# Kernel optimization log

Measured on AMD Instinct MI355X. Metric: run time of the kernel, lower is better.

The kernel has to match this reference:

```python
import jax, jax.numpy as jnp
import numpy as np

B, S, D = 4, 4096, 256

def setup_inputs() -> dict:
    key = jax.random.key(0)
    k1, k2, k3, k4 = jax.random.split(key, 4)
    inputs = jax.random.normal(k1, (B, S, D), dtype=jnp.float32)
    Wq = jax.random.normal(k2, (D, D), dtype=jnp.float32) * 0.05
    Wk = jax.random.normal(k3, (D, D), dtype=jnp.float32) * 0.05
    Wv = jax.random.normal(k4, (D, D), dtype=jnp.float32) * 0.05
    return {"inputs": inputs, "Wq": Wq, "Wk": Wk, "Wv": Wv}

def reference(inputs, Wq, Wk, Wv):
    # single-head self-attention: softmax(QK^T / sqrt(d)) V
    d = inputs.shape[-1]
    Q = jnp.einsum('bsd,de->bse', inputs, Wq)
    K = jnp.einsum('bsd,de->bse', inputs, Wk)
    V = jnp.einsum('bsd,de->bse', inputs, Wv)
    scale = 1.0 / jnp.sqrt(jnp.asarray(d, dtype=inputs.dtype))
    scores = jnp.einsum('bqe,bke->bqk', Q, K) * scale  # [B,S,S]
    attn = jax.nn.softmax(scores, axis=-1)
    return jnp.einsum('bqk,bke->bqe', attn, V)
```

## Files before the change

### kernel.cpp

```cpp
#include <hip/hip_runtime.h>
#include <hip/hip_bf16.h>

typedef __attribute__((ext_vector_type(8))) short bfrag_t;
typedef __attribute__((ext_vector_type(4))) float facc_t;
typedef __attribute__((ext_vector_type(16))) float f16acc_t;
typedef __attribute__((ext_vector_type(4))) int i4_t;

#define B_ 4
#define S_ 4096
#define D_ 256

using gas_v = const __attribute__((address_space(1))) void;
using las_v = __attribute__((address_space(3))) void;

__device__ __forceinline__ short f2bf(float f) {
  union { float fv; unsigned u; } x; x.fv = f;
  unsigned r = x.u + 0x7FFFu + ((x.u >> 16) & 1u);
  return (short)(r >> 16);
}

__device__ __forceinline__ int cvtpk(float lo, float hi) {
  int r;
  asm("v_cvt_pk_bf16_f32 %0, %1, %2" : "=v"(r) : "v"(lo), "v"(hi));
  return r;
}

__device__ __forceinline__ facc_t mfma16(bfrag_t a, bfrag_t b, facc_t c) {
  return __builtin_amdgcn_mfma_f32_16x16x32_bf16(a, b, c, 0, 0, 0);
}
__device__ __forceinline__ f16acc_t mfma32(bfrag_t a, bfrag_t b, f16acc_t c) {
  return __builtin_amdgcn_mfma_f32_32x32x16_bf16(a, b, c, 0, 0, 0);
}

__global__ void wt_kernel(const float* __restrict__ Wq, const float* __restrict__ Wk,
                          const float* __restrict__ Wv, short* __restrict__ WT) {
  const int p = blockIdx.x >> 4;
  const float* W = (p == 0) ? Wq : ((p == 1) ? Wk : Wv);
  short* o = WT + p * (D_ * D_);
  const int e = (blockIdx.x & 15) * 16 + (threadIdx.x >> 4);
  const int td = threadIdx.x & 15;
  #pragma unroll
  for (int dd = 0; dd < 16; ++dd) {
    int d = td * 16 + dd;
    o[e * D_ + d] = f2bf(W[d * D_ + e]);
  }
}

__global__ __launch_bounds__(256) void proj_kernel(
    const float* __restrict__ X, const short* __restrict__ WT,
    short* __restrict__ Qb, short* __restrict__ Kb, short* __restrict__ VT) {
  __shared__ __align__(16) short Vt[256 * 72];
  const int tid  = threadIdx.x;
  const int wave = tid >> 6, lane = tid & 63;
  const int lrow = lane & 15, kch = lane >> 4;
  const int p  = blockIdx.x >> 8;
  const int rb = blockIdx.x & 255;
  const int row0 = rb * 64 + wave * 16;
  const int arow = row0 + lrow;
  const int bblk = rb >> 6;

  bfrag_t af[8];
  #pragma unroll
  for (int kt = 0; kt < 8; ++kt) {
    const float* src = X + (size_t)arow * D_ + kt * 32 + kch * 8;
    float4 a = *reinterpret_cast<const float4*>(src);
    float4 b = *reinterpret_cast<const float4*>(src + 4);
    bfrag_t f;
    f[0] = f2bf(a.x); f[1] = f2bf(a.y); f[2] = f2bf(a.z); f[3] = f2bf(a.w);
    f[4] = f2bf(b.x); f[5] = f2bf(b.y); f[6] = f2bf(b.z); f[7] = f2bf(b.w);
    af[kt] = f;
  }

  const short* Wp = WT + p * (D_ * D_);
  facc_t acc[16];
  #pragma unroll
  for (int nt = 0; nt < 16; ++nt) acc[nt] = (facc_t)0.0f;
  #pragma unroll
  for (int kt = 0; kt < 8; ++kt) {
    #pragma unroll
    for (int nt = 0; nt < 16; ++nt) {
      bfrag_t bf = *reinterpret_cast<const bfrag_t*>(
          Wp + (nt * 16 + lrow) * D_ + kt * 32 + kch * 8);
      acc[nt] = mfma16(af[kt], bf, acc[nt]);
    }
  }
  if (p == 0) {
    #pragma unroll
    for (int nt = 0; nt < 16; ++nt)
      #pragma unroll
      for (int r = 0; r < 4; ++r)
        Qb[(size_t)(row0 + kch * 4 + r) * D_ + nt * 16 + lrow] =
            f2bf(acc[nt][r] * 0.0625f);
  } else if (p == 1) {
    #pragma unroll
    for (int nt = 0; nt < 16; ++nt)
      #pragma unroll
      for (int r = 0; r < 4; ++r)
        Kb[(size_t)(row0 + kch * 4 + r) * D_ + nt * 16 + lrow] = f2bf(acc[nt][r]);
  } else {
    #pragma unroll
    for (int nt = 0; nt < 16; ++nt)
      #pragma unroll
      for (int r = 0; r < 4; ++r)
        Vt[(nt * 16 + lrow) * 72 + (wave >> 1) * 32 + (wave & 1) * 16 +
           (kch & 1) * 8 + (kch >> 1) * 4 + r] = f2bf(acc[nt][r]);
    __syncthreads();
    const int d = tid;
    const int s0 = (rb & 63) * 64;
    short* dst = VT + ((size_t)(bblk * D_ + d)) * S_ + s0;
    #pragma unroll
    for (int j = 0; j < 8; ++j)
      *reinterpret_cast<bfrag_t*>(dst + j * 8) =
          *reinterpret_cast<const bfrag_t*>(&Vt[d * 72 + j * 8]);
  }
}

template<int SPLIT>
__global__ __launch_bounds__(256, 2) void attn32(
    const short* __restrict__ Qb, const short* __restrict__ Kb,
    const short* __restrict__ VT, float* __restrict__ P0,
    float* __restrict__ PX, float2* __restrict__ ML) {
  __shared__ __align__(16) short Kl[2][32 * 256];
  __shared__ __align__(16) short Vl[2][256 * 32];
  const int tid  = threadIdx.x;
  const int wave = tid >> 6, lane = tid & 63;
  const int l31 = lane & 31, hi = lane >> 5;
  const int ksw = (lane & 7) << 4;
  const int vsw = ((l31 >> 1) & 3) << 4;
  const int hw = blockIdx.x;
  const int g = hw & 7, rest = hw >> 3;
  int b, part, qblk;
  if constexpr (SPLIT == 4)      { b = g >> 1; part = (g & 1) * 2 + (rest & 1); qblk = rest >> 1; }
  else if constexpr (SPLIT == 2) { b = g >> 1; part = g & 1;                    qblk = rest; }
  else                           { b = g >> 1; part = 0;                qblk = (g & 1) * 16 + rest; }
  const int q0 = qblk * 128 + wave * 32;
  const int kvbase = part * (S_ / SPLIT);
  constexpr int STEPS = (S_ / SPLIT) / 32;

  const short* Kbp = Kb + (size_t)b * S_ * D_ + (size_t)kvbase * D_;
  const short* Vbp = VT + (size_t)b * D_ * S_ + kvbase;

  bfrag_t qf[16];
  const short* Qp = Qb + ((size_t)b * S_ + q0 + l31) * D_;
  #pragma unroll
  for (int kt = 0; kt < 16; ++kt)
    qf[kt] = *reinterpret_cast<const bfrag_t*>(Qp + kt * 16 + hi * 8);

  auto stage = [&](int bf, int kv0) {
    #pragma unroll
    for (int j = 0; j < 4; ++j) {
      int L = j * 4096 + tid * 16;
      int row = L >> 9;
      int cs = (L & 511) ^ ((row & 7) << 4);
      const short* src = Kbp + (size_t)(kv0 + row) * D_ + (cs >> 1);
      short* dst = &Kl[bf][(j * 4096 + wave * 1024) >> 1];
      __builtin_amdgcn_global_load_lds((gas_v*)src, (las_v*)dst, 16, 0, 0);
    }
    #pragma unroll
    for (int j = 0; j < 4; ++j) {
      int L = j * 4096 + tid * 16;
      int d = L >> 6;
      int cs = (L & 63) ^ (((d >> 1) & 3) << 4);
      const short* src = Vbp + (size_t)d * S_ + kv0 + (cs >> 1);
      short* dst = &Vl[bf][(j * 4096 + wave * 1024) >> 1];
      __builtin_amdgcn_global_load_lds((gas_v*)src, (las_v*)dst, 16, 0, 0);
    }
  };

  f16acc_t o32[8];
  #pragma unroll
  for (int nt = 0; nt < 8; ++nt) o32[nt] = (f16acc_t)0.0f;
  float mrow = -3.0e38f, lsum = 0.0f;

  stage(0, 0);
  asm volatile("s_waitcnt vmcnt(0)" ::: "memory");
  __syncthreads();
  int buf = 0;

  #pragma unroll 1
  for (int t = 0; t < STEPS; ++t) {
    if (t < STEPS - 1) stage(buf ^ 1, (t + 1) * 32);
    f16acc_t s16 = (f16acc_t)0.0f;
    const char* Kbase = (const char*)&Kl[buf][0];
    __builtin_amdgcn_s_setprio(1);
    #pragma unroll
    for (int kt = 0; kt < 16; ++kt) {
      bfrag_t kf = *reinterpret_cast<const bfrag_t*>(
          Kbase + l31 * 512 + ((kt * 32 + hi * 16) ^ ksw));
      s16 = mfma32(kf, qf[kt], s16);
    }
    __builtin_amdgcn_s_setprio(0);
    float mx = s16[0];
    #pragma unroll
    for (int i = 1; i < 16; ++i) mx = fmaxf(mx, s16[i]);
    mx = fmaxf(mx, __shfl_xor(mx, 32));
    if (mx > mrow + 8.0f) {
      float sf = __expf(mrow - mx);
      mrow = mx;
      lsum *= sf;
      #pragma unroll
      for (int nt = 0; nt < 8; ++nt) o32[nt] *= sf;
    }
    float pe[16];
    float ls = 0.0f;
    #pragma unroll
    for (int i = 0; i < 16; ++i) {
      pe[i] = __expf(s16[i] - mrow);
      ls += pe[i];
    }
    lsum += ls;
    i4_t w0, w1;
    w0.x = cvtpk(pe[0], pe[1]);  w0.y = cvtpk(pe[2], pe[3]);
    w0.z = cvtpk(pe[4], pe[5]);  w0.w = cvtpk(pe[6], pe[7]);
    w1.x = cvtpk(pe[8], pe[9]);  w1.y = cvtpk(pe[10], pe[11]);
    w1.z = cvtpk(pe[12], pe[13]); w1.w = cvtpk(pe[14], pe[15]);
    bfrag_t pb0 = __builtin_bit_cast(bfrag_t, w0);
    bfrag_t pb1 = __builtin_bit_cast(bfrag_t, w1);
    const char* Vbase = (const char*)&Vl[buf][0];
    __builtin_amdgcn_s_setprio(1);
    #pragma unroll
    for (int nt = 0; nt < 8; ++nt) {
      const char* vb = Vbase + (nt * 32 + l31) * 64;
      bfrag_t v0 = *reinterpret_cast<const bfrag_t*>(vb + ((hi * 16) ^ vsw));
      o32[nt] = mfma32(v0, pb0, o32[nt]);
      bfrag_t v1 = *reinterpret_cast<const bfrag_t*>(vb + ((32 + hi * 16) ^ vsw));
      o32[nt] = mfma32(v1, pb1, o32[nt]);
    }
    __builtin_amdgcn_s_setprio(0);
    asm volatile("s_waitcnt vmcnt(0)" ::: "memory");
    __syncthreads();
    buf ^= 1;
  }

  lsum += __shfl_xor(lsum, 32);
  float* Pd = (SPLIT == 1 || part == 0)
                  ? P0 : PX + (size_t)(part - 1) * ((size_t)B_ * S_ * D_);
  float* Og = Pd + ((size_t)b * S_ + q0 + l31) * D_;
  if constexpr (SPLIT == 1) {
    float inv = 1.0f / lsum;
    #pragma unroll
    for (int nt = 0; nt < 8; ++nt)
      #pragma unroll
      for (int gg = 0; gg < 4; ++gg) {
        float4 o;
        o.x = o32[nt][gg * 4 + 0] * inv; o.y = o32[nt][gg * 4 + 1] * inv;
        o.z = o32[nt][gg * 4 + 2] * inv; o.w = o32[nt][gg * 4 + 3] * inv;
        *reinterpret_cast<float4*>(Og + nt * 32 + hi * 4 + gg * 8) = o;
      }
  } else {
    #pragma unroll
    for (int nt = 0; nt < 8; ++nt)
      #pragma unroll
      for (int gg = 0; gg < 4; ++gg) {
        float4 o;
        o.x = o32[nt][gg * 4 + 0]; o.y = o32[nt][gg * 4 + 1];
        o.z = o32[nt][gg * 4 + 2]; o.w = o32[nt][gg * 4 + 3];
        *reinterpret_cast<float4*>(Og + nt * 32 + hi * 4 + gg * 8) = o;
      }
    if (lane < 32) {
      float2 ml; ml.x = mrow; ml.y = lsum;
      ML[part * (B_ * S_) + b * S_ + q0 + l31] = ml;
    }
  }
}

template<int SPLIT>
__global__ __launch_bounds__(256) void combineN(
    const float* __restrict__ PX, const float2* __restrict__ ML,
    float* __restrict__ Out) {
  const int r = blockIdx.x * 4 + (threadIdx.x >> 6);
  const int d4 = (threadIdx.x & 63) * 4;
  float2 ml[SPLIT];
  #pragma unroll
  for (int p = 0; p < SPLIT; ++p) ml[p] = ML[p * (B_ * S_) + r];
  float m = ml[0].x;
  #pragma unroll
  for (int p = 1; p < SPLIT; ++p) m = fmaxf(m, ml[p].x);
  float w[SPLIT];
  float denom = 0.0f;
  #pragma unroll
  for (int p = 0; p < SPLIT; ++p) {
    w[p] = __expf(ml[p].x - m);
    denom += ml[p].y * w[p];
  }
  float inv = 1.0f / denom;
  size_t idx = (size_t)r * D_ + d4;
  float4 x = *reinterpret_cast<float4*>(Out + idx);
  float4 acc;
  acc.x = x.x * w[0]; acc.y = x.y * w[0]; acc.z = x.z * w[0]; acc.w = x.w * w[0];
  #pragma unroll
  for (int p = 1; p < SPLIT; ++p) {
    float4 y = *reinterpret_cast<const float4*>(
        PX + (size_t)(p - 1) * ((size_t)B_ * S_ * D_) + idx);
    acc.x += y.x * w[p]; acc.y += y.y * w[p];
    acc.z += y.z * w[p]; acc.w += y.w * w[p];
  }
  acc.x *= inv; acc.y *= inv; acc.z *= inv; acc.w *= inv;
  *reinterpret_cast<float4*>(Out + idx) = acc;
}

extern "C" void kernel_launch(void* const* d_in, const int* in_sizes, int n_in,
                              void* d_out, int out_size, void* d_ws, size_t ws_size,
                              hipStream_t stream) {
  const float* X  = (const float*)d_in[0];
  const float* Wq = (const float*)d_in[1];
  const float* Wk = (const float*)d_in[2];
  const float* Wv = (const float*)d_in[3];
  float* out = (float*)d_out;

  char* ws = (char*)d_ws;
  short* Qb = (short*)(ws);
  short* Kb = (short*)(ws + 8388608);
  short* VT = (short*)(ws + 16777216);
  short* WT = (short*)(ws + 25165824);
  float2* ML = (float2*)(ws + 25690112);
  float* PX  = (float*)(ws + 26214400);
  const size_t NP = (size_t)B_ * S_ * D_ * 4;
  const size_t need4 = 26214400 + 3 * NP;
  const size_t need2 = 26214400 + 1 * NP;

  wt_kernel<<<48, 256, 0, stream>>>(Wq, Wk, Wv, WT);
  proj_kernel<<<768, 256, 0, stream>>>(X, WT, Qb, Kb, VT);
  if (ws_size >= need4) {
    attn32<4><<<512, 256, 0, stream>>>(Qb, Kb, VT, out, PX, ML);
    combineN<4><<<(B_ * S_) / 4, 256, 0, stream>>>(PX, ML, out);
  } else if (ws_size >= need2) {
    attn32<2><<<256, 256, 0, stream>>>(Qb, Kb, VT, out, PX, ML);
    combineN<2><<<(B_ * S_) / 4, 256, 0, stream>>>(PX, ML, out);
  } else {
    attn32<1><<<128, 256, 0, stream>>>(Qb, Kb, VT, out, PX, (float2*)out);
  }
}
```

Measured before the change: 160.0 us.

## Triple-buffer attention KV staging with 512-thread blocks and fuse QKV projection per block

The attention kernel now runs 8 waves per block over 256 query rows, sharing each staged K/V tile across twice as many waves. K/V staging becomes a triple-buffered ring with a partial vmcnt wait and a single barrier per step, and the block-to-work mapping across XCDs is reorganised. The projection kernel computes Q, K and V in one block per row tile, reusing the converted X fragments, and writes Q/K through LDS as coalesced 16-byte stores. The trade-off is more LDS per block (three buffers), which may reduce occupancy, and fewer projection blocks.

After: 157.0 us. About the same (-1.9%).

```diff
diff --git a/kernel.cpp b/kernel.cpp
--- a/kernel.cpp
+++ b/kernel.cpp
@@ -2,6 +2,7 @@
 #include <hip/hip_bf16.h>
 
 typedef __attribute__((ext_vector_type(8))) short bfrag_t;
+typedef __attribute__((ext_vector_type(4))) short s4_t;
 typedef __attribute__((ext_vector_type(4))) float facc_t;
 typedef __attribute__((ext_vector_type(16))) float f16acc_t;
 typedef __attribute__((ext_vector_type(4))) int i4_t;
@@ -49,12 +50,11 @@
 __global__ __launch_bounds__(256) void proj_kernel(
     const float* __restrict__ X, const short* __restrict__ WT,
     short* __restrict__ Qb, short* __restrict__ Kb, short* __restrict__ VT) {
-  __shared__ __align__(16) short Vt[256 * 72];
+  __shared__ __align__(16) short Stg[256 * 72];
   const int tid  = threadIdx.x;
   const int wave = tid >> 6, lane = tid & 63;
   const int lrow = lane & 15, kch = lane >> 4;
-  const int p  = blockIdx.x >> 8;
-  const int rb = blockIdx.x & 255;
+  const int rb = blockIdx.x;
   const int row0 = rb * 64 + wave * 16;
   const int arow = row0 + lrow;
   const int bblk = rb >> 6;
@@ -71,69 +71,85 @@
     af[kt] = f;
   }
 
-  const short* Wp = WT + p * (D_ * D_);
-  facc_t acc[16];
-  #pragma unroll
-  for (int nt = 0; nt < 16; ++nt) acc[nt] = (facc_t)0.0f;
-  #pragma unroll
-  for (int kt = 0; kt < 8; ++kt) {
-    #pragma unroll
-    for (int nt = 0; nt < 16; ++nt) {
-      bfrag_t bf = *reinterpret_cast<const bfrag_t*>(
-          Wp + (nt * 16 + lrow) * D_ + kt * 32 + kch * 8);
-      acc[nt] = mfma16(af[kt], bf, acc[nt]);
-    }
-  }
-  if (p == 0) {
-    #pragma unroll
-    for (int nt = 0; nt < 16; ++nt)
-      #pragma unroll
-      for (int r = 0; r < 4; ++r)
-        Qb[(size_t)(row0 + kch * 4 + r) * D_ + nt * 16 + lrow] =
-            f2bf(acc[nt][r] * 0.0625f);
-  } else if (p == 1) {
-    #pragma unroll
-    for (int nt = 0; nt < 16; ++nt)
-      #pragma unroll
-      for (int r = 0; r < 4; ++r)
-        Kb[(size_t)(row0 + kch * 4 + r) * D_ + nt * 16 + lrow] = f2bf(acc[nt][r]);
-  } else {
-    #pragma unroll
-    for (int nt = 0; nt < 16; ++nt)
-      #pragma unroll
-      for (int r = 0; r < 4; ++r)
-        Vt[(nt * 16 + lrow) * 72 + (wave >> 1) * 32 + (wave & 1) * 16 +
-           (kch & 1) * 8 + (kch >> 1) * 4 + r] = f2bf(acc[nt][r]);
+  #pragma unroll 1
+  for (int p = 0; p < 3; ++p) {
+    const short* Wp = WT + p * (D_ * D_);
+    facc_t acc[16];
+    #pragma unroll
+    for (int nt = 0; nt < 16; ++nt) acc[nt] = (facc_t)0.0f;
+    #pragma unroll
+    for (int kt = 0; kt < 8; ++kt) {
+      #pragma unroll
+      for (int nt = 0; nt < 16; ++nt) {
+        bfrag_t bf = *reinterpret_cast<const bfrag_t*>(
+            Wp + (nt * 16 + lrow) * D_ + kt * 32 + kch * 8);
+        acc[nt] = mfma16(af[kt], bf, acc[nt]);
+      }
+    }
     __syncthreads();
-    const int d = tid;
-    const int s0 = (rb & 63) * 64;
-    short* dst = VT + ((size_t)(bblk * D_ + d)) * S_ + s0;
-    #pragma unroll
-    for (int j = 0; j < 8; ++j)
-      *reinterpret_cast<bfrag_t*>(dst + j * 8) =
-          *reinterpret_cast<const bfrag_t*>(&Vt[d * 72 + j * 8]);
+    if (p < 2) {
+      const float sc = (p == 0) ? 0.0625f : 1.0f;
+      #pragma unroll
+      for (int nt = 0; nt < 16; ++nt)
+        #pragma unroll
+        for (int r = 0; r < 4; ++r)
+          Stg[(wave * 16 + kch * 4 + r) * 264 + nt * 16 + lrow] =
+              f2bf(acc[nt][r] * sc);
+      __syncthreads();
+      short* dstbase = ((p == 0) ? Qb : Kb) + (size_t)rb * 64 * D_;
+      #pragma unroll
+      for (int k = 0; k < 8; ++k) {
+        int c = k * 256 + tid;
+        int row = c >> 5, col = c & 31;
+        *reinterpret_cast<bfrag_t*>(dstbase + row * D_ + col * 8) =
+            *reinterpret_cast<const bfrag_t*>(&Stg[row * 264 + col * 8]);
+      }
+    } else {
+      #pragma unroll
+      for (int nt = 0; nt < 16; ++nt) {
+        s4_t v;
+        #pragma unroll
+        for (int r = 0; r < 4; ++r) v[r] = f2bf(acc[nt][r]);
+        *reinterpret_cast<s4_t*>(
+            &Stg[(nt * 16 + lrow) * 72 + (wave >> 1) * 32 + (wave & 1) * 16 +
+                 (kch & 1) * 8 + (kch >> 1) * 4]) = v;
+      }
+      __syncthreads();
+      const int d = tid;
+      const int s0 = (rb & 63) * 64;
+      short* dst = VT + ((size_t)(bblk * D_ + d)) * S_ + s0;
+      #pragma unroll
+      for (int j = 0; j < 8; ++j)
+        *reinterpret_cast<bfrag_t*>(dst + j * 8) =
+            *reinterpret_cast<const bfrag_t*>(&Stg[d * 72 + j * 8]);
+    }
   }
 }
 
 template<int SPLIT>
-__global__ __launch_bounds__(256, 2) void attn32(
+__global__ __launch_bounds__(512, 2) void attn32(
     const short* __restrict__ Qb, const short* __restrict__ Kb,
     const short* __restrict__ VT, float* __restrict__ P0,
     float* __restrict__ PX, float2* __restrict__ ML) {
-  __shared__ __align__(16) short Kl[2][32 * 256];
-  __shared__ __align__(16) short Vl[2][256 * 32];
+  __shared__ __align__(16) short Kl[3][32 * 256];
+  __shared__ __align__(16) short Vl[3][256 * 32];
   const int tid  = threadIdx.x;
   const int wave = tid >> 6, lane = tid & 63;
   const int l31 = lane & 31, hi = lane >> 5;
   const int ksw = (lane & 7) << 4;
   const int vsw = ((l31 >> 1) & 3) << 4;
   const int hw = blockIdx.x;
-  const int g = hw & 7, rest = hw >> 3;
+  const int xcd = hw & 7, i = hw >> 3;
   int b, part, qblk;
-  if constexpr (SPLIT == 4)      { b = g >> 1; part = (g & 1) * 2 + (rest & 1); qblk = rest >> 1; }
-  else if constexpr (SPLIT == 2) { b = g >> 1; part = g & 1;                    qblk = rest; }
-  else                           { b = g >> 1; part = 0;                qblk = (g & 1) * 16 + rest; }
-  const int q0 = qblk * 128 + wave * 32;
+  if constexpr (SPLIT == 4) {
+    int combo = (i & 1) * 8 + xcd;
+    b = combo >> 2; part = combo & 3; qblk = i >> 1;
+  } else if constexpr (SPLIT == 2) {
+    b = xcd >> 1; part = xcd & 1; qblk = i;
+  } else {
+    b = hw >> 4; part = 0; qblk = hw & 15;
+  }
+  const int q0 = qblk * 256 + wave * 32;
   const int kvbase = part * (S_ / SPLIT);
   constexpr int STEPS = (S_ / SPLIT) / 32;
 
@@ -148,21 +164,21 @@
 
   auto stage = [&](int bf, int kv0) {
     #pragma unroll
-    for (int j = 0; j < 4; ++j) {
-      int L = j * 4096 + tid * 16;
+    for (int j = 0; j < 2; ++j) {
+      int L = j * 8192 + tid * 16;
       int row = L >> 9;
       int cs = (L & 511) ^ ((row & 7) << 4);
       const short* src = Kbp + (size_t)(kv0 + row) * D_ + (cs >> 1);
-      short* dst = &Kl[bf][(j * 4096 + wave * 1024) >> 1];
+      short* dst = &Kl[bf][(j * 8192 + wave * 1024) >> 1];
       __builtin_amdgcn_global_load_lds((gas_v*)src, (las_v*)dst, 16, 0, 0);
     }
     #pragma unroll
-    for (int j = 0; j < 4; ++j) {
-      int L = j * 4096 + tid * 16;
+    for (int j = 0; j < 2; ++j) {
+      int L = j * 8192 + tid * 16;
       int d = L >> 6;
       int cs = (L & 63) ^ (((d >> 1) & 3) << 4);
       const short* src = Vbp + (size_t)d * S_ + kv0 + (cs >> 1);
-      short* dst = &Vl[bf][(j * 4096 + wave * 1024) >> 1];
+      short* dst = &Vl[bf][(j * 8192 + wave * 1024) >> 1];
       __builtin_amdgcn_global_load_lds((gas_v*)src, (las_v*)dst, 16, 0, 0);
     }
   };
@@ -173,13 +189,20 @@
   float mrow = -3.0e38f, lsum = 0.0f;
 
   stage(0, 0);
-  asm volatile("s_waitcnt vmcnt(0)" ::: "memory");
-  __syncthreads();
-  int buf = 0;
+  stage(1, 32);
 
   #pragma unroll 1
   for (int t = 0; t < STEPS; ++t) {
-    if (t < STEPS - 1) stage(buf ^ 1, (t + 1) * 32);
+    const int buf = t % 3;
+    if (t < STEPS - 1) {
+      asm volatile("s_waitcnt vmcnt(4)" ::: "memory");
+    } else {
+      asm volatile("s_waitcnt vmcnt(0)" ::: "memory");
+    }
+    __builtin_amdgcn_sched_barrier(0);
+    __builtin_amdgcn_s_barrier();
+    __builtin_amdgcn_sched_barrier(0);
+    if (t + 2 < STEPS) stage((t + 2) % 3, (t + 2) * 32);
     f16acc_t s16 = (f16acc_t)0.0f;
     const char* Kbase = (const char*)&Kl[buf][0];
     __builtin_amdgcn_s_setprio(1);
@@ -192,7 +215,7 @@
     __builtin_amdgcn_s_setprio(0);
     float mx = s16[0];
     #pragma unroll
-    for (int i = 1; i < 16; ++i) mx = fmaxf(mx, s16[i]);
+    for (int i2 = 1; i2 < 16; ++i2) mx = fmaxf(mx, s16[i2]);
     mx = fmaxf(mx, __shfl_xor(mx, 32));
     if (mx > mrow + 8.0f) {
       float sf = __expf(mrow - mx);
@@ -201,19 +224,19 @@
       #pragma unroll
       for (int nt = 0; nt < 8; ++nt) o32[nt] *= sf;
     }
-    float pe[16];
     float ls = 0.0f;
     #pragma unroll
-    for (int i = 0; i < 16; ++i) {
-      pe[i] = __expf(s16[i] - mrow);
-      ls += pe[i];
+    for (int i2 = 0; i2 < 16; ++i2) {
+      float e = __expf(s16[i2] - mrow);
+      s16[i2] = e;
+      ls += e;
     }
     lsum += ls;
     i4_t w0, w1;
-    w0.x = cvtpk(pe[0], pe[1]);  w0.y = cvtpk(pe[2], pe[3]);
-    w0.z = cvtpk(pe[4], pe[5]);  w0.w = cvtpk(pe[6], pe[7]);
-    w1.x = cvtpk(pe[8], pe[9]);  w1.y = cvtpk(pe[10], pe[11]);
-    w1.z = cvtpk(pe[12], pe[13]); w1.w = cvtpk(pe[14], pe[15]);
+    w0.x = cvtpk(s16[0], s16[1]);   w0.y = cvtpk(s16[2], s16[3]);
+    w0.z = cvtpk(s16[4], s16[5]);   w0.w = cvtpk(s16[6], s16[7]);
+    w1.x = cvtpk(s16[8], s16[9]);   w1.y = cvtpk(s16[10], s16[11]);
+    w1.z = cvtpk(s16[12], s16[13]); w1.w = cvtpk(s16[14], s16[15]);
     bfrag_t pb0 = __builtin_bit_cast(bfrag_t, w0);
     bfrag_t pb1 = __builtin_bit_cast(bfrag_t, w1);
     const char* Vbase = (const char*)&Vl[buf][0];
@@ -227,9 +250,6 @@
       o32[nt] = mfma32(v1, pb1, o32[nt]);
     }
     __builtin_amdgcn_s_setprio(0);
-    asm volatile("s_waitcnt vmcnt(0)" ::: "memory");
-    __syncthreads();
-    buf ^= 1;
   }
 
   lsum += __shfl_xor(lsum, 32);
@@ -320,14 +340,14 @@
   const size_t need2 = 26214400 + 1 * NP;
 
   wt_kernel<<<48, 256, 0, stream>>>(Wq, Wk, Wv, WT);
-  proj_kernel<<<768, 256, 0, stream>>>(X, WT, Qb, Kb, VT);
+  proj_kernel<<<256, 256, 0, stream>>>(X, WT, Qb, Kb, VT);
   if (ws_size >= need4) {
-    attn32<4><<<512, 256, 0, stream>>>(Qb, Kb, VT, out, PX, ML);
+    attn32<4><<<256, 512, 0, stream>>>(Qb, Kb, VT, out, PX, ML);
     combineN<4><<<(B_ * S_) / 4, 256, 0, stream>>>(PX, ML, out);
   } else if (ws_size >= need2) {
-    attn32<2><<<256, 256, 0, stream>>>(Qb, Kb, VT, out, PX, ML);
+    attn32<2><<<128, 512, 0, stream>>>(Qb, Kb, VT, out, PX, ML);
     combineN<2><<<(B_ * S_) / 4, 256, 0, stream>>>(PX, ML, out);
   } else {
-    attn32<1><<<128, 256, 0, stream>>>(Qb, Kb, VT, out, PX, (float2*)out);
-  }
-}
+    attn32<1><<<64, 512, 0, stream>>>(Qb, Kb, VT, out, PX, (float2*)out);
+  }
+}
```
